# Performance work log

Measured on AMD Instinct MI355X. Metric: run time of the kernel, lower is better.

The kernel has to match this reference:

```python
import jax, jax.numpy as jnp
import numpy as np

N_NODES = 100000
N_EDGES = 640000
EMB = 128
BATCH = 16384
N_REL = 2
HIDDEN = [128, 64, 32]
LN_EPS = 1e-5
NORM_EPS = 1e-12


def setup_inputs() -> dict:
    key = jax.random.key(0)
    ks = jax.random.split(key, 24)
    inp = {}
    inp["user_indices"] = jax.random.randint(ks[0], (BATCH,), 0, N_NODES)
    inp["item_indices"] = jax.random.randint(ks[1], (BATCH,), 0, N_NODES)
    inp["edge_index"] = jax.random.randint(ks[2], (2, N_EDGES), 0, N_NODES)
    inp["edge_type"] = jax.random.randint(ks[3], (N_EDGES,), 0, N_REL)
    inp["edge_weight"] = jax.random.uniform(ks[4], (N_EDGES,), dtype=jnp.float32)
    # parameters
    s = 1.0 / np.sqrt(EMB)
    inp["embedding"] = jax.random.normal(ks[5], (N_NODES, EMB), jnp.float32) * 0.02
    inp["w1_rel"] = jax.random.normal(ks[6], (N_REL, EMB, EMB), jnp.float32) * s
    inp["w1_root"] = jax.random.normal(ks[7], (EMB, EMB), jnp.float32) * s
    inp["b1"] = jnp.zeros((EMB,), jnp.float32)
    inp["ln_g"] = jnp.ones((EMB,), jnp.float32)
    inp["ln_b"] = jnp.zeros((EMB,), jnp.float32)
    inp["w2_rel"] = jax.random.normal(ks[8], (N_REL, EMB, EMB), jnp.float32) * s
    inp["w2_root"] = jax.random.normal(ks[9], (EMB, EMB), jnp.float32) * s
    inp["b2"] = jnp.zeros((EMB,), jnp.float32)
    dims = [2 * EMB] + HIDDEN
    for i in range(len(HIDDEN)):
        inp[f"mlp_w{i}"] = jax.random.normal(ks[10 + i], (dims[i], dims[i + 1]), jnp.float32) / np.sqrt(dims[i])
        inp[f"mlp_b{i}"] = jnp.zeros((dims[i + 1],), jnp.float32)
    d_out = HIDDEN[-1] + EMB
    inp["out_w"] = jax.random.normal(ks[20], (d_out, 1), jnp.float32) / np.sqrt(d_out)
    inp["out_b"] = jnp.zeros((1,), jnp.float32)
    return inp


def rgcn_layer(x, edge_index, edge_type, edge_weight, w_rel, w_root, bias):
    # x: [N, D]; edge_index: [2, E]; per-relation linear on gathered source feats,
    # weighted scatter-add into destination nodes, plus root transform + bias.
    src, dst = edge_index[0], edge_index[1]
    x_j = x[src]  # [E, D] gather
    msg = jnp.zeros((x_j.shape[0], w_rel.shape[2]), x.dtype)
    for r in range(w_rel.shape[0]):  # small fixed relation count
        msg = msg + jnp.where((edge_type == r)[:, None], x_j @ w_rel[r], 0.0)
    msg = msg * edge_weight[:, None]
    agg = jax.ops.segment_sum(msg, dst, num_segments=x.shape[0])
    return agg + x @ w_root + bias


def layer_norm(x, g, b):
    mu = jnp.mean(x, axis=-1, keepdims=True)
    var = jnp.mean(jnp.square(x - mu), axis=-1, keepdims=True)
    return (x - mu) * jax.lax.rsqrt(var + LN_EPS) * g + b


def l2_normalize(x):
    n = jnp.sqrt(jnp.sum(jnp.square(x), axis=-1, keepdims=True))
    return x / jnp.maximum(n, NORM_EPS)


def reference(user_indices, item_indices, edge_index, edge_type, edge_weight,
              embedding, w1_rel, w1_root, b1, ln_g, ln_b, w2_rel, w2_root, b2,
              mlp_w0, mlp_b0, mlp_w1, mlp_b1, mlp_w2, mlp_b2, out_w, out_b):
    x = embedding  # embedding(arange(N)) == full table
    x = rgcn_layer(x, edge_index, edge_type, edge_weight, w1_rel, w1_root, b1)
    x = jax.nn.relu(x)
    # dropout is identity in eval mode
    x = layer_norm(x, ln_g, ln_b)
    x = rgcn_layer(x, edge_index, edge_type, edge_weight, w2_rel, w2_root, b2)

    u = x[user_indices]  # [B, D]
    v = x[item_indices]
    gmf = l2_normalize(u) * l2_normalize(v)  # [B, D]
    h = jnp.concatenate([u, v], axis=-1)  # [B, 2D]
    for w, b in ((mlp_w0, mlp_b0), (mlp_w1, mlp_b1), (mlp_w2, mlp_b2)):
        h = jax.nn.relu(h @ w + b)
    final = jnp.concatenate([gmf, h], axis=-1)  # [B, D + 32]
    score = jax.nn.sigmoid(final @ out_w + out_b)
    return jnp.squeeze(score, axis=-1)
```

## Files before the change

### kernel.cpp

```cpp
#include <hip/hip_runtime.h>
#include <cstddef>
#include <cstdint>

#define N_NODES 100000
#define N_EDGES 640000
#define EMBD    128
#define NBATCH  16384
#define CHUNK   1024
#define NCHUNK  ((N_NODES + CHUNK - 1) / CHUNK)
#define BELEMS  49152

typedef short bf16x8 __attribute__((ext_vector_type(8)));
typedef float f32x4  __attribute__((ext_vector_type(4)));

__device__ __forceinline__ unsigned pack_split(float x) {
    unsigned u  = __float_as_uint(x);
    unsigned hi = (u + 0x7fffu + ((u >> 16) & 1u)) & 0xffff0000u;
    float    lo = x - __uint_as_float(hi);
    unsigned ul = __float_as_uint(lo);
    unsigned lw = ((ul + 0x7fffu + ((ul >> 16) & 1u)) >> 16) & 0xffffu;
    return hi | lw;
}
__device__ __forceinline__ float bf2f(unsigned short h) {
    return __uint_as_float((unsigned)h << 16);
}

__global__ __launch_bounds__(256) void pack_hist(
    const float* __restrict__ emb,
    unsigned short* __restrict__ xH, unsigned short* __restrict__ xL,
    const int* __restrict__ ei, int* __restrict__ cursor,
    const int* __restrict__ ui, const int* __restrict__ vi,
    int* __restrict__ flag, int* __restrict__ nlist, int* __restrict__ count,
    const float* __restrict__ w1rel, const float* __restrict__ w1root,
    const float* __restrict__ w2rel, const float* __restrict__ w2root,
    unsigned short* __restrict__ BpH, unsigned short* __restrict__ BpL,
    int n2, int E)
{
    const int j = blockIdx.x * 256 + threadIdx.x;
    if (j < n2) {
        const float2 v = ((const float2*)emb)[j];
        const unsigned p0 = pack_split(v.x);
        const unsigned p1 = pack_split(v.y);
        ((unsigned*)xH)[j] = (p1 & 0xffff0000u) | (p0 >> 16);
        ((unsigned*)xL)[j] = (p1 << 16) | (p0 & 0xffffu);
    }
    if (j < E) atomicAdd(&cursor[ei[E + j]], 1);
    if (j < 2 * NBATCH) {
        const int idx = (j < NBATCH) ? ui[j] : vi[j - NBATCH];
        if (atomicExch(&flag[idx], 1) == 0)
            nlist[atomicAdd(count, 1)] = idx;
    }
    if (j < 2 * BELEMS) {
        const int lay = (j >= BELEMS);
        const int q   = j - lay * BELEMS;
        const int p   = q >> 14;
        const int rem = q & 16383;
        const int k   = rem >> 7;
        const int c   = rem & 127;
        const float* wr = lay ? w2rel : w1rel;
        const float* wo = lay ? w2root : w1root;
        const float v = (p < 2) ? wr[(size_t)(p * 128 + k) * 128 + c]
                                : wo[(size_t)k * 128 + c];
        const unsigned ps = pack_split(v);
        const int kc   = p * 4 + (k >> 5);
        const int half = (k >> 4) & 1;
        const int jj   = k & 15;
        const size_t dst = ((size_t)(kc * 2 + half) * 128 + c) * 16 + jj;
        BpH[(size_t)lay * BELEMS + dst] = (unsigned short)(ps >> 16);
        BpL[(size_t)lay * BELEMS + dst] = (unsigned short)(ps & 0xffffu);
    }
}

__global__ __launch_bounds__(256) void scan_local(
    int* __restrict__ cursor, int* __restrict__ bsum, int n)
{
    __shared__ int part[256];
    const int t    = threadIdx.x;
    const int base = blockIdx.x * CHUNK + t * 4;
    int v[4];
    int s = 0;
#pragma unroll
    for (int i = 0; i < 4; ++i) {
        const int idx = base + i;
        v[i] = (idx < n) ? cursor[idx] : 0;
        s += v[i];
    }
    part[t] = s;
    __syncthreads();
    for (int off = 1; off < 256; off <<= 1) {
        const int add = (t >= off) ? part[t - off] : 0;
        __syncthreads();
        part[t] += add;
        __syncthreads();
    }
    if (t == 255) bsum[blockIdx.x] = part[255];
    int run = (t == 0) ? 0 : part[t - 1];
#pragma unroll
    for (int i = 0; i < 4; ++i) {
        const int idx = base + i;
        if (idx < n) { cursor[idx] = run; run += v[i]; }
    }
}

__global__ __launch_bounds__(256) void scan_add(
    int* __restrict__ cursor, const int* __restrict__ bsum, int n)
{
    __shared__ int red[256];
    const int t = threadIdx.x;
    const int b = blockIdx.x;
    red[t] = (t < b && t < NCHUNK) ? bsum[t] : 0;
    __syncthreads();
    for (int off = 128; off > 0; off >>= 1) {
        if (t < off) red[t] += red[t + off];
        __syncthreads();
    }
    const int off_ = red[0];
    const int base = b * CHUNK + t * 4;
#pragma unroll
    for (int i = 0; i < 4; ++i) {
        const int idx = base + i;
        if (idx < n) cursor[idx] += off_;
    }
}

__global__ __launch_bounds__(256) void bucket_kernel(
    const int* __restrict__ ei, const int* __restrict__ et,
    const float* __restrict__ ew, int* __restrict__ cursor,
    int2* __restrict__ srec, int E)
{
    const int e = blockIdx.x * 256 + threadIdx.x;
    if (e >= E) return;
    const int src = ei[e];
    const int dst = ei[E + e];
    const int r   = et[e];
    const int pos = atomicAdd(&cursor[dst], 1);
    srec[pos] = make_int2(src | (r << 17), __float_as_int(ew[e]));
}

__device__ __forceinline__ void accum_node(
    const unsigned short* __restrict__ xh, const int2* __restrict__ srec,
    const int* __restrict__ cursor,
    unsigned short* __restrict__ AH, unsigned short* __restrict__ AL,
    int wid, int lane, int N)
{
    const int s = (wid == 0) ? 0 : cursor[wid - 1];
    const int e = cursor[wid];

    float ax = 0.f, ay = 0.f, bx = 0.f, by = 0.f;
    int i = s;
    for (; i + 3 < e; i += 4) {
        const int2 r0 = srec[i];
        const int2 r1 = srec[i + 1];
        const int2 r2 = srec[i + 2];
        const int2 r3 = srec[i + 3];
        const unsigned g0 = ((const unsigned*)(xh + (size_t)(r0.x & 0x1FFFF) * EMBD))[lane];
        const unsigned g1 = ((const unsigned*)(xh + (size_t)(r1.x & 0x1FFFF) * EMBD))[lane];
        const unsigned g2 = ((const unsigned*)(xh + (size_t)(r2.x & 0x1FFFF) * EMBD))[lane];
        const unsigned g3 = ((const unsigned*)(xh + (size_t)(r3.x & 0x1FFFF) * EMBD))[lane];
        const float w0 = __int_as_float(r0.y);
        const float w1 = __int_as_float(r1.y);
        const float w2 = __int_as_float(r2.y);
        const float w3 = __int_as_float(r3.y);
        {
            const float vx = bf2f((unsigned short)(g0 & 0xffffu));
            const float vy = bf2f((unsigned short)(g0 >> 16));
            if (r0.x & (1 << 17)) { bx += vx * w0; by += vy * w0; }
            else                  { ax += vx * w0; ay += vy * w0; }
        }
        {
            const float vx = bf2f((unsigned short)(g1 & 0xffffu));
            const float vy = bf2f((unsigned short)(g1 >> 16));
            if (r1.x & (1 << 17)) { bx += vx * w1; by += vy * w1; }
            else                  { ax += vx * w1; ay += vy * w1; }
        }
        {
            const float vx = bf2f((unsigned short)(g2 & 0xffffu));
            const float vy = bf2f((unsigned short)(g2 >> 16));
            if (r2.x & (1 << 17)) { bx += vx * w2; by += vy * w2; }
            else                  { ax += vx * w2; ay += vy * w2; }
        }
        {
            const float vx = bf2f((unsigned short)(g3 & 0xffffu));
            const float vy = bf2f((unsigned short)(g3 >> 16));
            if (r3.x & (1 << 17)) { bx += vx * w3; by += vy * w3; }
            else                  { ax += vx * w3; ay += vy * w3; }
        }
    }
    for (; i < e; ++i) {
        const int2 r0 = srec[i];
        const unsigned g0 = ((const unsigned*)(xh + (size_t)(r0.x & 0x1FFFF) * EMBD))[lane];
        const float w0 = __int_as_float(r0.y);
        const float vx = bf2f((unsigned short)(g0 & 0xffffu));
        const float vy = bf2f((unsigned short)(g0 >> 16));
        if (r0.x & (1 << 17)) { bx += vx * w0; by += vy * w0; }
        else                  { ax += vx * w0; ay += vy * w0; }
    }
    const unsigned pax = pack_split(ax), pay = pack_split(ay);
    const unsigned pbx = pack_split(bx), pby = pack_split(by);
    ((unsigned*)(AH + (size_t)wid * EMBD))[lane]       = (pay & 0xffff0000u) | (pax >> 16);
    ((unsigned*)(AL + (size_t)wid * EMBD))[lane]       = (pay << 16) | (pax & 0xffffu);
    ((unsigned*)(AH + ((size_t)N + wid) * EMBD))[lane] = (pby & 0xffff0000u) | (pbx >> 16);
    ((unsigned*)(AL + ((size_t)N + wid) * EMBD))[lane] = (pby << 16) | (pbx & 0xffffu);
}

__global__ __launch_bounds__(256) void accum_csr(
    const unsigned short* __restrict__ xh, const int2* __restrict__ srec,
    const int* __restrict__ cursor,
    unsigned short* __restrict__ AH, unsigned short* __restrict__ AL, int N)
{
    const int wid = blockIdx.x * 4 + (threadIdx.x >> 6);
    accum_node(xh, srec, cursor, AH, AL, wid, threadIdx.x & 63, N);
}

__global__ __launch_bounds__(256) void accum_csr_list(
    const unsigned short* __restrict__ xh, const int2* __restrict__ srec,
    const int* __restrict__ cursor, const int* __restrict__ nlist,
    const int* __restrict__ count,
    unsigned short* __restrict__ AH, unsigned short* __restrict__ AL, int N)
{
    const int wi = blockIdx.x * 4 + (threadIdx.x >> 6);
    if (wi >= *count) return;
    accum_node(xh, srec, cursor, AH, AL, nlist[wi], threadIdx.x & 63, N);
}

__global__ __launch_bounds__(256) void gemm_mfma(
    const unsigned short* __restrict__ S0H, const unsigned short* __restrict__ S0L,
    const unsigned short* __restrict__ S1H, const unsigned short* __restrict__ S1L,
    const unsigned short* __restrict__ S2H, const unsigned short* __restrict__ S2L,
    const unsigned short* __restrict__ BpH, const unsigned short* __restrict__ BpL,
    const float* __restrict__ bias, const float* __restrict__ lng,
    const float* __restrict__ lnb,
    unsigned short* __restrict__ outH, unsigned short* __restrict__ outL,
    const int* __restrict__ rowlist, const int* __restrict__ rowcnt,
    int M, int do_ln)
{
    __shared__ unsigned short AsH[128 * 40], AsL[128 * 40];
    __shared__ unsigned short BsH[128 * 40], BsL[128 * 40];
    __shared__ float lnbuf[2][128][2];
    __shared__ int rows[128];

    const int t    = threadIdx.x;
    const int wave = t >> 6;
    const int lane = t & 63;
    const int q    = lane >> 4;
    const int n    = lane & 15;
    const int wrow = wave & 1;
    const int wcol = wave >> 1;
    const int m0   = blockIdx.x * 128;

    const int cnt = rowcnt ? *rowcnt : M;
    if (m0 >= cnt) return;
    if (t < 128) {
        const int rr = m0 + t;
        rows[t] = (rr < cnt) ? (rowlist ? rowlist[rr] : rr) : -1;
    }
    __syncthreads();

    const int arow  = t >> 1;
    const int ahalf = t & 1;
    const int bcol  = t & 127;
    const int bkh   = t >> 7;

    f32x4 acc[4][4];
#pragma unroll
    for (int rt = 0; rt < 4; ++rt)
#pragma unroll
        for (int ct = 0; ct < 4; ++ct)
            acc[rt][ct] = (f32x4){0.f, 0.f, 0.f, 0.f};

    uint4 au0, au1, au2, au3;
    uint4 bu0, bu1, bu2, bu3;
    auto loadA = [&](int kc) {
        const unsigned short* SH = (kc < 4) ? S0H : (kc < 8) ? S1H : S2H;
        const unsigned short* SL = (kc < 4) ? S0L : (kc < 8) ? S1L : S2L;
        const int node = rows[arow];
        if (node >= 0) {
            const size_t off = (size_t)node * EMBD + (kc & 3) * 32 + ahalf * 16;
            au0 = *(const uint4*)(SH + off);
            au1 = *(const uint4*)(SH + off + 8);
            au2 = *(const uint4*)(SL + off);
            au3 = *(const uint4*)(SL + off + 8);
        } else {
            au0 = au1 = au2 = au3 = make_uint4(0u, 0u, 0u, 0u);
        }
    };
    auto loadB = [&](int kc) {
        const size_t off = ((size_t)(kc * 2 + bkh) * 128 + bcol) * 16;
        bu0 = *(const uint4*)(BpH + off);
        bu1 = *(const uint4*)(BpH + off + 8);
        bu2 = *(const uint4*)(BpL + off);
        bu3 = *(const uint4*)(BpL + off + 8);
    };

    loadA(0);
    loadB(0);

    for (int kc = 0; kc < 12; ++kc) {
        __syncthreads();

        {
            uint4* pH = (uint4*)(AsH + arow * 40 + ahalf * 16);
            uint4* pL = (uint4*)(AsL + arow * 40 + ahalf * 16);
            pH[0] = au0; pH[1] = au1;
            pL[0] = au2; pL[1] = au3;
            uint4* qH = (uint4*)(BsH + bcol * 40 + bkh * 16);
            uint4* qL = (uint4*)(BsL + bcol * 40 + bkh * 16);
            qH[0] = bu0; qH[1] = bu1;
            qL[0] = bu2; qL[1] = bu3;
        }

        if (kc < 11) { loadA(kc + 1); loadB(kc + 1); }
        __syncthreads();

        bf16x8 ah[4], al[4];
#pragma unroll
        for (int rt = 0; rt < 4; ++rt) {
            const int r = wrow * 64 + rt * 16 + n;
            ah[rt] = *(const bf16x8*)&AsH[r * 40 + q * 8];
            al[rt] = *(const bf16x8*)&AsL[r * 40 + q * 8];
        }
#pragma unroll
        for (int ct = 0; ct < 4; ++ct) {
            const int c = wcol * 64 + ct * 16 + n;
            const bf16x8 bh = *(const bf16x8*)&BsH[c * 40 + q * 8];
            const bf16x8 bl = *(const bf16x8*)&BsL[c * 40 + q * 8];
#pragma unroll
            for (int rt = 0; rt < 4; ++rt) {
                acc[rt][ct] = __builtin_amdgcn_mfma_f32_16x16x32_bf16(ah[rt], bh, acc[rt][ct], 0, 0, 0);
                acc[rt][ct] = __builtin_amdgcn_mfma_f32_16x16x32_bf16(ah[rt], bl, acc[rt][ct], 0, 0, 0);
                acc[rt][ct] = __builtin_amdgcn_mfma_f32_16x16x32_bf16(al[rt], bh, acc[rt][ct], 0, 0, 0);
            }
        }
    }

    float bb[4], gg[4], tb[4];
#pragma unroll
    for (int ct = 0; ct < 4; ++ct) {
        const int c = wcol * 64 + ct * 16 + n;
        bb[ct] = bias[c];
        gg[ct] = do_ln ? lng[c] : 0.f;
        tb[ct] = do_ln ? lnb[c] : 0.f;
    }

    if (do_ln) {
#pragma unroll
        for (int rt = 0; rt < 4; ++rt)
#pragma unroll
            for (int r = 0; r < 4; ++r) {
                float s = 0.f, sq = 0.f;
#pragma unroll
                for (int ct = 0; ct < 4; ++ct) {
                    float v = acc[rt][ct][r] + bb[ct];
                    v = fmaxf(v, 0.f);
                    acc[rt][ct][r] = v;
                    s += v; sq += v * v;
                }
#pragma unroll
                for (int off = 1; off < 16; off <<= 1) {
                    s  += __shfl_xor(s,  off, 64);
                    sq += __shfl_xor(sq, off, 64);
                }
                if (n == 0) {
                    const int row = wrow * 64 + rt * 16 + q * 4 + r;
                    lnbuf[wcol][row][0] = s;
                    lnbuf[wcol][row][1] = sq;
                }
            }
        __syncthreads();
#pragma unroll
        for (int rt = 0; rt < 4; ++rt)
#pragma unroll
            for (int r = 0; r < 4; ++r) {
                const int row  = wrow * 64 + rt * 16 + q * 4 + r;
                const int node = rows[row];
                const float s    = lnbuf[0][row][0] + lnbuf[1][row][0];
                const float sq   = lnbuf[0][row][1] + lnbuf[1][row][1];
                const float mu   = s * (1.0f / 128.0f);
                const float var  = sq * (1.0f / 128.0f) - mu * mu;
                const float rstd = rsqrtf(var + 1e-5f);
                if (node >= 0) {
#pragma unroll
                    for (int ct = 0; ct < 4; ++ct) {
                        const int c = wcol * 64 + ct * 16 + n;
                        const float v = (acc[rt][ct][r] - mu) * rstd * gg[ct] + tb[ct];
                        const unsigned p = pack_split(v);
                        outH[(size_t)node * EMBD + c] = (unsigned short)(p >> 16);
                        outL[(size_t)node * EMBD + c] = (unsigned short)(p & 0xffffu);
                    }
                }
            }
    } else {
#pragma unroll
        for (int rt = 0; rt < 4; ++rt)
#pragma unroll
            for (int r = 0; r < 4; ++r) {
                const int node = rows[wrow * 64 + rt * 16 + q * 4 + r];
                if (node >= 0) {
#pragma unroll
                    for (int ct = 0; ct < 4; ++ct) {
                        const int c = wcol * 64 + ct * 16 + n;
                        const unsigned p = pack_split(acc[rt][ct][r] + bb[ct]);
                        outH[(size_t)node * EMBD + c] = (unsigned short)(p >> 16);
                        outL[(size_t)node * EMBD + c] = (unsigned short)(p & 0xffffu);
                    }
                }
            }
    }
}

__global__ __launch_bounds__(256) void head_kernel(
    const unsigned short* __restrict__ x2H, const unsigned short* __restrict__ x2L,
    const int* __restrict__ ui, const int* __restrict__ vi,
    const float* __restrict__ mw0, const float* __restrict__ mb0,
    const float* __restrict__ mw1, const float* __restrict__ mb1,
    const float* __restrict__ mw2, const float* __restrict__ mb2,
    const float* __restrict__ ow, const float* __restrict__ ob,
    float* __restrict__ out, int B)
{
    __shared__ float h0[16][256];
    __shared__ float h1[16][128];
    __shared__ float h2[16][64];
    __shared__ float h3[16][32];
    __shared__ float ps_u[16][16], ps_v[16][16];
    __shared__ float inv_nunv[16];
    __shared__ float pg[16][16], ph[16][16];

    const int t   = threadIdx.x;
    const int bb0 = blockIdx.x * 16;

    for (int r = 0; r < 16; ++r) {
        const int b   = bb0 + r;
        const int idx = (t < 128) ? ui[b] : vi[b];
        const int c   = t & 127;
        const size_t o = (size_t)idx * EMBD + c;
        h0[r][t] = bf2f(x2H[o]) + bf2f(x2L[o]);
    }
    __syncthreads();

    {
        const int row = t >> 4, sub = t & 15;
        float su = 0.f, sv = 0.f;
#pragma unroll
        for (int k = 0; k < 8; ++k) {
            const float a = h0[row][sub + 16 * k];       su += a * a;
            const float b = h0[row][128 + sub + 16 * k]; sv += b * b;
        }
        ps_u[row][sub] = su; ps_v[row][sub] = sv;
    }
    __syncthreads();
    if (t < 16) {
        float su = 0.f, sv = 0.f;
#pragma unroll
        for (int k = 0; k < 16; ++k) { su += ps_u[t][k]; sv += ps_v[t][k]; }
        const float nu = fmaxf(sqrtf(su), 1e-12f);
        const float nv = fmaxf(sqrtf(sv), 1e-12f);
        inv_nunv[t] = 1.0f / (nu * nv);
    }
    __syncthreads();

    {
        const int c = t & 127, rr = t >> 7;
        float acc[8];
#pragma unroll
        for (int j = 0; j < 8; ++j) acc[j] = 0.f;
        for (int i = 0; i < 256; i += 4) {
            const float w0 = mw0[(i + 0) * 128 + c];
            const float w1 = mw0[(i + 1) * 128 + c];
            const float w2 = mw0[(i + 2) * 128 + c];
            const float w3 = mw0[(i + 3) * 128 + c];
#pragma unroll
            for (int j = 0; j < 8; ++j) {
                const float4 a = *(const float4*)&h0[rr * 8 + j][i];
                acc[j] += a.x * w0 + a.y * w1 + a.z * w2 + a.w * w3;
            }
        }
        const float bv = mb0[c];
#pragma unroll
        for (int j = 0; j < 8; ++j) h1[rr * 8 + j][c] = fmaxf(acc[j] + bv, 0.f);
    }
    __syncthreads();

    {
        const int c = t & 63, g = t >> 6;
        float acc[4] = {0.f, 0.f, 0.f, 0.f};
        for (int i = 0; i < 128; i += 4) {
            const float w0 = mw1[(i + 0) * 64 + c];
            const float w1 = mw1[(i + 1) * 64 + c];
            const float w2 = mw1[(i + 2) * 64 + c];
            const float w3 = mw1[(i + 3) * 64 + c];
#pragma unroll
            for (int j = 0; j < 4; ++j) {
                const float4 a = *(const float4*)&h1[g * 4 + j][i];
                acc[j] += a.x * w0 + a.y * w1 + a.z * w2 + a.w * w3;
            }
        }
        const float bv = mb1[c];
#pragma unroll
        for (int j = 0; j < 4; ++j) h2[g * 4 + j][c] = fmaxf(acc[j] + bv, 0.f);
    }
    __syncthreads();

    {
        const int c = t & 31, g = t >> 5;
        float acc[2] = {0.f, 0.f};
        for (int i = 0; i < 64; i += 4) {
            const float w0 = mw2[(i + 0) * 32 + c];
            const float w1 = mw2[(i + 1) * 32 + c];
            const float w2 = mw2[(i + 2) * 32 + c];
            const float w3 = mw2[(i + 3) * 32 + c];
#pragma unroll
            for (int j = 0; j < 2; ++j) {
                const float4 a = *(const float4*)&h2[g * 2 + j][i];
                acc[j] += a.x * w0 + a.y * w1 + a.z * w2 + a.w * w3;
            }
        }
        const float bv = mb2[c];
#pragma unroll
        for (int j = 0; j < 2; ++j) h3[g * 2 + j][c] = fmaxf(acc[j] + bv, 0.f);
    }
    __syncthreads();

    {
        const int row = t >> 4, sub = t & 15;
        float pgv = 0.f;
#pragma unroll
        for (int k = 0; k < 8; ++k) {
            const int c = sub + 16 * k;
            pgv += h0[row][c] * h0[row][128 + c] * ow[c];
        }
        const float phv = h3[row][sub]      * ow[128 + sub]
                        + h3[row][sub + 16] * ow[144 + sub];
        pg[row][sub] = pgv; ph[row][sub] = phv;
    }
    __syncthreads();
    if (t < 16) {
        float sg = 0.f, sh = 0.f;
#pragma unroll
        for (int k = 0; k < 16; ++k) { sg += pg[t][k]; sh += ph[t][k]; }
        const float z = sg * inv_nunv[t] + sh + ob[0];
        out[bb0 + t] = 1.0f / (1.0f + expf(-z));
    }
}

extern "C" void kernel_launch(void* const* d_in, const int* in_sizes, int n_in,
                              void* d_out, int out_size, void* d_ws, size_t ws_size,
                              hipStream_t stream)
{
    const int*   ui      = (const int*)d_in[0];
    const int*   vi      = (const int*)d_in[1];
    const int*   ei      = (const int*)d_in[2];
    const int*   et      = (const int*)d_in[3];
    const float* ew      = (const float*)d_in[4];
    const float* emb     = (const float*)d_in[5];
    const float* w1_rel  = (const float*)d_in[6];
    const float* w1_root = (const float*)d_in[7];
    const float* b1      = (const float*)d_in[8];
    const float* ln_g    = (const float*)d_in[9];
    const float* ln_b    = (const float*)d_in[10];
    const float* w2_rel  = (const float*)d_in[11];
    const float* w2_root = (const float*)d_in[12];
    const float* b2      = (const float*)d_in[13];
    const float* mw0     = (const float*)d_in[14];
    const float* mb0     = (const float*)d_in[15];
    const float* mw1     = (const float*)d_in[16];
    const float* mb1     = (const float*)d_in[17];
    const float* mw2     = (const float*)d_in[18];
    const float* mb2     = (const float*)d_in[19];
    const float* ow      = (const float*)d_in[20];
    const float* ob      = (const float*)d_in[21];
    float* out = (float*)d_out;

    const int N = N_NODES, E = N_EDGES, B = NBATCH;

    unsigned short* aggH = (unsigned short*)d_ws;
    unsigned short* aggL = aggH + (size_t)2 * N * EMBD;
    unsigned short* xH   = aggL + (size_t)2 * N * EMBD;
    unsigned short* xL   = xH + (size_t)N * EMBD;
    int2*           srec = (int2*)(xL + (size_t)N * EMBD);
    unsigned short* BpH  = (unsigned short*)(srec + E);
    unsigned short* BpL  = BpH + (size_t)2 * BELEMS;
    int*            cursor = (int*)(BpL + (size_t)2 * BELEMS);
    int*            flag   = cursor + N;
    int*            count  = flag + N;
    int*            bsum   = count + 1;
    int*            nlist  = bsum + NCHUNK;

    hipMemsetAsync(cursor, 0, (size_t)(2 * N + 1) * sizeof(int), stream);
    pack_hist<<<(N * EMBD / 2 + 255) / 256, 256, 0, stream>>>(
        emb, xH, xL, ei, cursor, ui, vi, flag, nlist, count,
        w1_rel, w1_root, w2_rel, w2_root, BpH, BpL,
        N * EMBD / 2, E);

    scan_local<<<NCHUNK, 256, 0, stream>>>(cursor, bsum, N);
    scan_add<<<NCHUNK, 256, 0, stream>>>(cursor, bsum, N);
    bucket_kernel<<<(E + 255) / 256, 256, 0, stream>>>(ei, et, ew, cursor, srec, E);

    accum_csr<<<N / 4, 256, 0, stream>>>(xH, srec, cursor, aggH, aggL, N);
    gemm_mfma<<<(N + 127) / 128, 256, 0, stream>>>(
        aggH, aggL, aggH + (size_t)N * EMBD, aggL + (size_t)N * EMBD, xH, xL,
        BpH, BpL, b1, ln_g, ln_b, xH, xL,
        nullptr, nullptr, N, 1);

    accum_csr_list<<<(2 * NBATCH) / 4, 256, 0, stream>>>(
        xH, srec, cursor, nlist, count, aggH, aggL, N);
    gemm_mfma<<<(2 * NBATCH + 127) / 128, 256, 0, stream>>>(
        aggH, aggL, aggH + (size_t)N * EMBD, aggL + (size_t)N * EMBD, xH, xL,
        BpH + BELEMS, BpL + BELEMS, b2, nullptr, nullptr, xH, xL,
        nlist, count, N, 0);

    head_kernel<<<B / 16, 256, 0, stream>>>(
        xH, xL, ui, vi, mw0, mb0, mw1, mb1, mw2, mb2, ow, ob, out, B);
}
```

Before: 464.2 us.

## Drop LDS staging in split-bf16 GEMM; load MFMA fragments directly from global

The GEMM no longer stages A and B tiles through shared memory with double-buffered register prefetch and two barriers per k-chunk. Each wave now loads its MFMA operand fragments straight from global memory, reading A rows per lane and B from a repacked weight layout of 32 contiguous k values per column. This removes the LDS writes, the barriers and the LDS bank traffic. In exchange each wave re-fetches data that was shared across waves, which relies on L2/L1 hits, and the software prefetch overlap with MFMA is lost.

Result: no change. 472.5 us (+1.8%).

```diff
diff --git a/kernel.cpp b/kernel.cpp
--- a/kernel.cpp
+++ b/kernel.cpp
@@ -62,10 +62,9 @@
         const float v = (p < 2) ? wr[(size_t)(p * 128 + k) * 128 + c]
                                 : wo[(size_t)k * 128 + c];
         const unsigned ps = pack_split(v);
-        const int kc   = p * 4 + (k >> 5);
-        const int half = (k >> 4) & 1;
-        const int jj   = k & 15;
-        const size_t dst = ((size_t)(kc * 2 + half) * 128 + c) * 16 + jj;
+        const int kc = p * 4 + (k >> 5);
+        const int kk = k & 31;
+        const size_t dst = ((size_t)kc * 128 + c) * 32 + kk;
         BpH[(size_t)lay * BELEMS + dst] = (unsigned short)(ps >> 16);
         BpL[(size_t)lay * BELEMS + dst] = (unsigned short)(ps & 0xffffu);
     }
@@ -234,8 +233,6 @@
     const int* __restrict__ rowlist, const int* __restrict__ rowcnt,
     int M, int do_ln)
 {
-    __shared__ unsigned short AsH[128 * 40], AsL[128 * 40];
-    __shared__ unsigned short BsH[128 * 40], BsL[128 * 40];
     __shared__ float lnbuf[2][128][2];
     __shared__ int rows[128];
 
@@ -256,10 +253,12 @@
     }
     __syncthreads();
 
-    const int arow  = t >> 1;
-    const int ahalf = t & 1;
-    const int bcol  = t & 127;
-    const int bkh   = t >> 7;
+    int nd[4];
+#pragma unroll
+    for (int rt = 0; rt < 4; ++rt) nd[rt] = rows[wrow * 64 + rt * 16 + n];
+
+    const int qo = q * 8;
+    const bf16x8 ZV = (bf16x8){0, 0, 0, 0, 0, 0, 0, 0};
 
     f32x4 acc[4][4];
 #pragma unroll
@@ -268,67 +267,39 @@
         for (int ct = 0; ct < 4; ++ct)
             acc[rt][ct] = (f32x4){0.f, 0.f, 0.f, 0.f};
 
-    uint4 au0, au1, au2, au3;
-    uint4 bu0, bu1, bu2, bu3;
-    auto loadA = [&](int kc) {
-        const unsigned short* SH = (kc < 4) ? S0H : (kc < 8) ? S1H : S2H;
-        const unsigned short* SL = (kc < 4) ? S0L : (kc < 8) ? S1L : S2L;
-        const int node = rows[arow];
-        if (node >= 0) {
-            const size_t off = (size_t)node * EMBD + (kc & 3) * 32 + ahalf * 16;
-            au0 = *(const uint4*)(SH + off);
-            au1 = *(const uint4*)(SH + off + 8);
-            au2 = *(const uint4*)(SL + off);
-            au3 = *(const uint4*)(SL + off + 8);
-        } else {
-            au0 = au1 = au2 = au3 = make_uint4(0u, 0u, 0u, 0u);
-        }
-    };
-    auto loadB = [&](int kc) {
-        const size_t off = ((size_t)(kc * 2 + bkh) * 128 + bcol) * 16;
-        bu0 = *(const uint4*)(BpH + off);
-        bu1 = *(const uint4*)(BpH + off + 8);
-        bu2 = *(const uint4*)(BpL + off);
-        bu3 = *(const uint4*)(BpL + off + 8);
-    };
-
-    loadA(0);
-    loadB(0);
-
-    for (int kc = 0; kc < 12; ++kc) {
-        __syncthreads();
-
-        {
-            uint4* pH = (uint4*)(AsH + arow * 40 + ahalf * 16);
-            uint4* pL = (uint4*)(AsL + arow * 40 + ahalf * 16);
-            pH[0] = au0; pH[1] = au1;
-            pL[0] = au2; pL[1] = au3;
-            uint4* qH = (uint4*)(BsH + bcol * 40 + bkh * 16);
-            uint4* qL = (uint4*)(BsL + bcol * 40 + bkh * 16);
-            qH[0] = bu0; qH[1] = bu1;
-            qL[0] = bu2; qL[1] = bu3;
-        }
-
-        if (kc < 11) { loadA(kc + 1); loadB(kc + 1); }
-        __syncthreads();
-
-        bf16x8 ah[4], al[4];
-#pragma unroll
-        for (int rt = 0; rt < 4; ++rt) {
-            const int r = wrow * 64 + rt * 16 + n;
-            ah[rt] = *(const bf16x8*)&AsH[r * 40 + q * 8];
-            al[rt] = *(const bf16x8*)&AsL[r * 40 + q * 8];
-        }
-#pragma unroll
-        for (int ct = 0; ct < 4; ++ct) {
-            const int c = wcol * 64 + ct * 16 + n;
-            const bf16x8 bh = *(const bf16x8*)&BsH[c * 40 + q * 8];
-            const bf16x8 bl = *(const bf16x8*)&BsL[c * 40 + q * 8];
+#pragma unroll
+    for (int src = 0; src < 3; ++src) {
+        const unsigned short* SH = (src == 0) ? S0H : (src == 1) ? S1H : S2H;
+        const unsigned short* SL = (src == 0) ? S0L : (src == 1) ? S1L : S2L;
+#pragma unroll
+        for (int k4 = 0; k4 < 4; ++k4) {
+            const int kc = src * 4 + k4;
+            const int ko = k4 * 32 + qo;
+
+            bf16x8 ah[4], al[4];
 #pragma unroll
             for (int rt = 0; rt < 4; ++rt) {
-                acc[rt][ct] = __builtin_amdgcn_mfma_f32_16x16x32_bf16(ah[rt], bh, acc[rt][ct], 0, 0, 0);
-                acc[rt][ct] = __builtin_amdgcn_mfma_f32_16x16x32_bf16(ah[rt], bl, acc[rt][ct], 0, 0, 0);
-                acc[rt][ct] = __builtin_amdgcn_mfma_f32_16x16x32_bf16(al[rt], bh, acc[rt][ct], 0, 0, 0);
+                if (nd[rt] >= 0) {
+                    const size_t ao = (size_t)nd[rt] * EMBD + ko;
+                    ah[rt] = *(const bf16x8*)(SH + ao);
+                    al[rt] = *(const bf16x8*)(SL + ao);
+                } else {
+                    ah[rt] = ZV;
+                    al[rt] = ZV;
+                }
+            }
+#pragma unroll
+            for (int ct = 0; ct < 4; ++ct) {
+                const int c = wcol * 64 + ct * 16 + n;
+                const size_t bo = ((size_t)kc * 128 + c) * 32 + qo;
+                const bf16x8 bh = *(const bf16x8*)(BpH + bo);
+                const bf16x8 bl = *(const bf16x8*)(BpL + bo);
+#pragma unroll
+                for (int rt = 0; rt < 4; ++rt) {
+                    acc[rt][ct] = __builtin_amdgcn_mfma_f32_16x16x32_bf16(ah[rt], bh, acc[rt][ct], 0, 0, 0);
+                    acc[rt][ct] = __builtin_amdgcn_mfma_f32_16x16x32_bf16(ah[rt], bl, acc[rt][ct], 0, 0, 0);
+                    acc[rt][ct] = __builtin_amdgcn_mfma_f32_16x16x32_bf16(al[rt], bh, acc[rt][ct], 0, 0, 0);
+                }
             }
         }
     }
```
